# Optimization experiments

Hardware: AMD Instinct MI355X
Metric: run time of the kernel (lower is better)

Reference implementation:

```python
import jax, jax.numpy as jnp
import numpy as np

N = 50000
E = 800000
IN_C, HID, OUT_C = 512, 256, 128


def gcn_conv(x, edge_index, W, b, num_nodes):
    # PyG GCNConv: add self-loops, symmetric normalization, linear-then-aggregate.
    h = x @ W  # [N, out]
    src = jnp.concatenate([edge_index[0], jnp.arange(num_nodes)])
    dst = jnp.concatenate([edge_index[1], jnp.arange(num_nodes)])
    ones = jnp.ones(src.shape[0], dtype=x.dtype)
    deg = jax.ops.segment_sum(ones, dst, num_segments=num_nodes)  # in-degree incl. self-loop
    dinv = jax.lax.rsqrt(deg)  # deg >= 1 thanks to self-loops
    norm = dinv[src] * dinv[dst]  # [E+N]
    msg = h[src] * norm[:, None]  # gather + scale
    out = jax.ops.segment_sum(msg, dst, num_segments=num_nodes)  # scatter-add
    return out + b


def setup_inputs() -> dict:
    key = jax.random.key(0)
    k_x, k_e, k_w1, k_b1, k_w2, k_b2 = jax.random.split(key, 6)
    x = jax.random.normal(k_x, (N, IN_C), dtype=jnp.float32)
    edge_index = jax.random.randint(k_e, (2, E), 0, N, dtype=jnp.int64)
    s1 = 1.0 / np.sqrt(IN_C)
    s2 = 1.0 / np.sqrt(HID)
    W1 = jax.random.uniform(k_w1, (IN_C, HID), jnp.float32, -s1, s1)
    b1 = jax.random.uniform(k_b1, (HID,), jnp.float32, -s1, s1)
    W2 = jax.random.uniform(k_w2, (HID, OUT_C), jnp.float32, -s2, s2)
    b2 = jax.random.uniform(k_b2, (OUT_C,), jnp.float32, -s2, s2)
    return {"x": x, "edge_index": edge_index, "W1": W1, "b1": b1, "W2": W2, "b2": b2}


def reference(x, edge_index, W1, b1, W2, b2):
    h = gcn_conv(x, edge_index, W1, b1, N)
    h = jax.nn.relu(h)
    # dropout in eval mode == identity
    return gcn_conv(h, edge_index, W2, b2, N)
```

## Files before the change

kernel.cpp:

```cpp
#include <hip/hip_runtime.h>
#include <stdint.h>

typedef __bf16 bf16_t;
typedef bf16_t bf16x8 __attribute__((ext_vector_type(8)));
typedef bf16_t bf16x4 __attribute__((ext_vector_type(4)));
typedef bf16_t bf16x2 __attribute__((ext_vector_type(2)));
typedef float  f32x4  __attribute__((ext_vector_type(4)));

typedef __attribute__((address_space(3))) void* as3p;
typedef const __attribute__((address_space(1))) void* as1p;

#define IN_C 512
#define HID  256
#define OUTC 128

__global__ void k_prep(const float* __restrict__ x, const float* __restrict__ W1,
                       const float* __restrict__ W2, const void* __restrict__ ei,
                       int* __restrict__ flag, int* __restrict__ cnt,
                       bf16_t* __restrict__ Xb, bf16_t* __restrict__ W1t,
                       bf16_t* __restrict__ W2t, int n, int mpad) {
  int t = blockIdx.x * blockDim.x + threadIdx.x;
  const int NC = mpad * 64;
  if (t < NC) {
    int r = t >> 6, c8 = t & 63;
    bf16x8 o;
    if (r < n) {
      const float4* px = (const float4*)(x + (size_t)r * IN_C);
      float4 a = px[c8 * 2];
      float4 b = px[c8 * 2 + 1];
      o[0] = (bf16_t)a.x; o[1] = (bf16_t)a.y; o[2] = (bf16_t)a.z; o[3] = (bf16_t)a.w;
      o[4] = (bf16_t)b.x; o[5] = (bf16_t)b.y; o[6] = (bf16_t)b.z; o[7] = (bf16_t)b.w;
    } else {
      for (int i = 0; i < 8; ++i) o[i] = (bf16_t)0.0f;
    }
    *(bf16x8*)(Xb + (size_t)r * IN_C + c8 * 8) = o;
    return;
  }
  int u = t - NC;
  if (u < IN_C * HID) {
    W1t[(size_t)(u & 255) * IN_C + (u >> 8)] = (bf16_t)W1[u];
    return;
  }
  u -= IN_C * HID;
  if (u < HID * OUTC) {
    W2t[(size_t)(u & 127) * HID + (u >> 7)] = (bf16_t)W2[u];
    return;
  }
  u -= HID * OUTC;
  if (u < n) {
    cnt[u] = 0;
    return;
  }
  if (u == n) {
    const long long* p = (const long long*)ei;
    int ok = 1;
    for (int i = 0; i < 64; ++i) {
      long long v = p[i];
      if (v < 0 || v >= n) ok = 0;
    }
    *flag = ok;
  }
}

__global__ void k_hist(const void* __restrict__ ei, const int* __restrict__ flag,
                       int* __restrict__ cnt, int E) {
  int e = blockIdx.x * blockDim.x + threadIdx.x;
  if (e >= E) return;
  int d;
  if (*flag) d = (int)((const long long*)ei)[(size_t)E + e];
  else       d = ((const int*)ei)[E + e];
  atomicAdd(&cnt[d], 1);
}

__global__ void k_scan1(const int* __restrict__ cnt, int* __restrict__ ex,
                        int* __restrict__ part, float* __restrict__ dinv, int n) {
  __shared__ int sh[256];
  int i = blockIdx.x * 256 + threadIdx.x;
  int v = (i < n) ? cnt[i] : 0;
  if (i < n) dinv[i] = rsqrtf((float)v + 1.0f);
  sh[threadIdx.x] = v;
  __syncthreads();
  int val = v;
  for (int off = 1; off < 256; off <<= 1) {
    int t = (threadIdx.x >= off) ? sh[threadIdx.x - off] : 0;
    __syncthreads();
    val += t;
    sh[threadIdx.x] = val;
    __syncthreads();
  }
  if (i < n) ex[i] = val - v;
  if (threadIdx.x == 255) part[blockIdx.x] = val;
}

__global__ void k_scan23(int* __restrict__ rs, const int* __restrict__ part,
                         int* __restrict__ cur, int n, int Etot) {
  __shared__ int sh[256];
  const int b = blockIdx.x, t = threadIdx.x;
  int p = 0;
  for (int j = t; j < b; j += 256) p += part[j];
  sh[t] = p;
  __syncthreads();
  for (int off = 128; off > 0; off >>= 1) {
    if (t < off) sh[t] += sh[t + off];
    __syncthreads();
  }
  int base = sh[0];
  int i = b * 256 + t;
  if (i < n) {
    int r = rs[i] + base;
    rs[i] = r;
    cur[i] = r;
  }
  if (i == 0) rs[n] = Etot;
}

__global__ void k_fill(const void* __restrict__ ei, const int* __restrict__ flag,
                       int* __restrict__ cur, int2* __restrict__ csrw,
                       const float* __restrict__ dinv, int E) {
  int e = blockIdx.x * blockDim.x + threadIdx.x;
  if (e >= E) return;
  int s, d;
  if (*flag) {
    const long long* p = (const long long*)ei;
    s = (int)p[e];
    d = (int)p[(size_t)E + e];
  } else {
    const int* p = (const int*)ei;
    s = p[e];
    d = p[E + e];
  }
  int pos = atomicAdd(&cur[d], 1);
  int2 v;
  v.x = s;
  v.y = __float_as_int(dinv[s]);
  csrw[pos] = v;
}

__global__ __launch_bounds__(256, 3) void k_gemm(const bf16_t* __restrict__ A,
                                                 const bf16_t* __restrict__ Bt,
                                                 bf16_t* __restrict__ C,
                                                 int Kdim, int Ncols) {
  __shared__ bf16_t As[128 * 32];
  __shared__ bf16_t Bs[128 * 32];
  const int bm = blockIdx.x, bn = blockIdx.y;
  const int tid = threadIdx.x;
  const int wave = tid >> 6, lane = tid & 63;
  const int wm = (wave >> 1) * 64, wn = (wave & 1) * 64;
  const int quad = lane >> 4, l16 = lane & 15;

  const size_t abase = (size_t)bm * 128 * Kdim;
  const size_t bbase = (size_t)bn * 128 * Kdim;

  f32x4 acc[4][4];
#pragma unroll
  for (int i = 0; i < 4; ++i)
#pragma unroll
    for (int j = 0; j < 4; ++j)
#pragma unroll
      for (int r = 0; r < 4; ++r) acc[i][j][r] = 0.0f;

  for (int kk = 0; kk < Kdim; kk += 32) {
#pragma unroll
    for (int i = 0; i < 2; ++i) {
      int g = i * 256 + tid;
      int row = g >> 2, col = (g & 3) * 8;
      const bf16_t* ga = A + abase + (size_t)row * Kdim + kk + col;
      __builtin_amdgcn_global_load_lds((as1p)ga,
                                       (as3p)(&As[(i * 256 + wave * 64) * 8]), 16, 0, 0);
      const bf16_t* gb = Bt + bbase + (size_t)row * Kdim + kk + col;
      __builtin_amdgcn_global_load_lds((as1p)gb,
                                       (as3p)(&Bs[(i * 256 + wave * 64) * 8]), 16, 0, 0);
    }
    __syncthreads();
    bf16x8 af[4], bf[4];
#pragma unroll
    for (int i = 0; i < 4; ++i)
      af[i] = *(const bf16x8*)(&As[(wm + i * 16 + l16) * 32 + quad * 8]);
#pragma unroll
    for (int j = 0; j < 4; ++j)
      bf[j] = *(const bf16x8*)(&Bs[(wn + j * 16 + l16) * 32 + quad * 8]);
#pragma unroll
    for (int i = 0; i < 4; ++i)
#pragma unroll
      for (int j = 0; j < 4; ++j)
        acc[i][j] = __builtin_amdgcn_mfma_f32_16x16x32_bf16(af[i], bf[j], acc[i][j], 0, 0, 0);
    __syncthreads();
  }

#pragma unroll
  for (int i = 0; i < 4; ++i) {
#pragma unroll
    for (int j = 0; j < 4; ++j) {
      int col = bn * 128 + wn + j * 16 + l16;
      int row0 = bm * 128 + wm + i * 16 + quad * 4;
#pragma unroll
      for (int r = 0; r < 4; ++r)
        C[(size_t)(row0 + r) * Ncols + col] = (bf16_t)acc[i][j][r];
    }
  }
}

__global__ void k_agg_l1(const bf16_t* __restrict__ H, const int* __restrict__ rs,
                         const int2* __restrict__ csrw, const float* __restrict__ dinv,
                         const float* __restrict__ b1, bf16_t* __restrict__ R,
                         int n, int mpad) {
  int d = blockIdx.x * 4 + (threadIdx.x >> 6);
  if (d >= mpad) return;
  int lane = threadIdx.x & 63;
  if (d >= n) {
    bf16x4 z;
    z[0] = (bf16_t)0.0f; z[1] = (bf16_t)0.0f; z[2] = (bf16_t)0.0f; z[3] = (bf16_t)0.0f;
    *(bf16x4*)(R + (size_t)d * HID + lane * 4) = z;
    return;
  }
  int e0 = rs[d], e1 = rs[d + 1];
  float acc[4][4];
  for (int k = 0; k < 4; ++k)
    for (int c = 0; c < 4; ++c) acc[k][c] = 0.f;
  int e = e0;
  for (; e + 8 <= e1; e += 8) {
    int2 cw[8];
    bf16x4 h[8];
#pragma unroll
    for (int u = 0; u < 8; ++u) cw[u] = csrw[e + u];
#pragma unroll
    for (int u = 0; u < 8; ++u)
      h[u] = *(const bf16x4*)(H + (size_t)cw[u].x * HID + lane * 4);
#pragma unroll
    for (int u = 0; u < 8; ++u) {
      float w = __int_as_float(cw[u].y);
#pragma unroll
      for (int c = 0; c < 4; ++c) acc[u & 3][c] += w * (float)h[u][c];
    }
  }
  for (; e < e1; ++e) {
    int2 cw = csrw[e];
    float w = __int_as_float(cw.y);
    bf16x4 hx = *(const bf16x4*)(H + (size_t)cw.x * HID + lane * 4);
#pragma unroll
    for (int c = 0; c < 4; ++c) acc[0][c] += w * (float)hx[c];
  }
  float dd = dinv[d];
  float dv2 = dd * dd;
  bf16x4 hs = *(const bf16x4*)(H + (size_t)d * HID + lane * 4);
  float4 bb = ((const float4*)b1)[lane];
  float a0 = (acc[0][0] + acc[1][0]) + (acc[2][0] + acc[3][0]);
  float a1 = (acc[0][1] + acc[1][1]) + (acc[2][1] + acc[3][1]);
  float a2 = (acc[0][2] + acc[1][2]) + (acc[2][2] + acc[3][2]);
  float a3 = (acc[0][3] + acc[1][3]) + (acc[2][3] + acc[3][3]);
  float v0 = fmaxf(a0 * dd + dv2 * (float)hs[0] + bb.x, 0.f);
  float v1 = fmaxf(a1 * dd + dv2 * (float)hs[1] + bb.y, 0.f);
  float v2 = fmaxf(a2 * dd + dv2 * (float)hs[2] + bb.z, 0.f);
  float v3 = fmaxf(a3 * dd + dv2 * (float)hs[3] + bb.w, 0.f);
  bf16x4 o;
  o[0] = (bf16_t)v0; o[1] = (bf16_t)v1; o[2] = (bf16_t)v2; o[3] = (bf16_t)v3;
  *(bf16x4*)(R + (size_t)d * HID + lane * 4) = o;
}

__global__ void k_agg_l2(const bf16_t* __restrict__ H, const int* __restrict__ rs,
                         const int2* __restrict__ csrw, const float* __restrict__ dinv,
                         const float* __restrict__ b2, float* __restrict__ out, int n) {
  int d = blockIdx.x * 4 + (threadIdx.x >> 6);
  if (d >= n) return;
  int lane = threadIdx.x & 63;
  int e0 = rs[d], e1 = rs[d + 1];
  float acc[4][2];
  for (int k = 0; k < 4; ++k) { acc[k][0] = 0.f; acc[k][1] = 0.f; }
  int e = e0;
  for (; e + 8 <= e1; e += 8) {
    int2 cw[8];
    bf16x2 h[8];
#pragma unroll
    for (int u = 0; u < 8; ++u) cw[u] = csrw[e + u];
#pragma unroll
    for (int u = 0; u < 8; ++u)
      h[u] = *(const bf16x2*)(H + (size_t)cw[u].x * OUTC + lane * 2);
#pragma unroll
    for (int u = 0; u < 8; ++u) {
      float w = __int_as_float(cw[u].y);
      acc[u & 3][0] += w * (float)h[u][0];
      acc[u & 3][1] += w * (float)h[u][1];
    }
  }
  for (; e < e1; ++e) {
    int2 cw = csrw[e];
    float w = __int_as_float(cw.y);
    bf16x2 hx = *(const bf16x2*)(H + (size_t)cw.x * OUTC + lane * 2);
    acc[0][0] += w * (float)hx[0];
    acc[0][1] += w * (float)hx[1];
  }
  float a0 = (acc[0][0] + acc[1][0]) + (acc[2][0] + acc[3][0]);
  float a1 = (acc[0][1] + acc[1][1]) + (acc[2][1] + acc[3][1]);
  float dd = dinv[d];
  float dv2 = dd * dd;
  bf16x2 hs = *(const bf16x2*)(H + (size_t)d * OUTC + lane * 2);
  float2 bb = ((const float2*)b2)[lane];
  float2 o;
  o.x = a0 * dd + dv2 * (float)hs[0] + bb.x;
  o.y = a1 * dd + dv2 * (float)hs[1] + bb.y;
  ((float2*)(out + (size_t)d * OUTC))[lane] = o;
}

extern "C" void kernel_launch(void* const* d_in, const int* in_sizes, int n_in,
                              void* d_out, int out_size, void* d_ws, size_t ws_size,
                              hipStream_t stream) {
  const float* x  = (const float*)d_in[0];
  const void*  ei = d_in[1];
  const float* W1 = (const float*)d_in[2];
  const float* b1 = (const float*)d_in[3];
  const float* W2 = (const float*)d_in[4];
  const float* b2 = (const float*)d_in[5];

  const int n = in_sizes[0] / IN_C;
  const int E = in_sizes[1] / 2;
  const int mpad = (n + 127) & ~127;

  char* w = (char*)d_ws;
  size_t off = 0;
  auto alloc = [&](size_t bytes) -> void* {
    void* p = w + off;
    off = (off + bytes + 255) & ~(size_t)255;
    return p;
  };

  int*    flag = (int*)alloc(4);
  int*    cnt  = (int*)alloc((size_t)n * 4);
  float*  dinv = (float*)alloc((size_t)n * 4);
  int*    rs   = (int*)alloc((size_t)(n + 1) * 4);
  int*    cur  = (int*)alloc((size_t)n * 4);
  int*    part = (int*)alloc(1024);
  int2*   csrw = (int2*)alloc((size_t)E * 8);
  bf16_t* Xb   = (bf16_t*)alloc((size_t)mpad * IN_C * 2);
  bf16_t* W1t  = (bf16_t*)alloc((size_t)HID * IN_C * 2);
  bf16_t* W2t  = (bf16_t*)alloc((size_t)OUTC * HID * 2);
  bf16_t* H1b  = (bf16_t*)alloc((size_t)mpad * HID * 2);
  bf16_t* R1b  = (bf16_t*)alloc((size_t)mpad * HID * 2);
  bf16_t* H2b  = (bf16_t*)alloc((size_t)mpad * OUTC * 2);
  (void)ws_size; (void)n_in; (void)out_size;

  const int nb = (n + 255) / 256;
  const int prepT = mpad * 64 + IN_C * HID + HID * OUTC + n + 1;

  k_prep<<<(prepT + 255) / 256, 256, 0, stream>>>(x, W1, W2, ei, flag, cnt,
                                                  Xb, W1t, W2t, n, mpad);
  k_hist<<<(E + 255) / 256, 256, 0, stream>>>(ei, flag, cnt, E);
  k_scan1<<<nb, 256, 0, stream>>>(cnt, rs, part, dinv, n);
  k_scan23<<<nb, 256, 0, stream>>>(rs, part, cur, n, E);
  k_fill<<<(E + 255) / 256, 256, 0, stream>>>(ei, flag, cur, csrw, dinv, E);

  k_gemm<<<dim3(mpad / 128, HID / 128), 256, 0, stream>>>(Xb, W1t, H1b, IN_C, HID);
  k_agg_l1<<<(mpad + 3) / 4, 256, 0, stream>>>(H1b, rs, csrw, dinv, b1, R1b, n, mpad);
  k_gemm<<<dim3(mpad / 128, OUTC / 128), 256, 0, stream>>>(R1b, W2t, H2b, HID, OUTC);
  k_agg_l2<<<(n + 3) / 4, 256, 0, stream>>>(H2b, rs, csrw, dinv, b2, (float*)d_out, n);
}
```

Baseline: 397.6 us.

## Fuse fp32-to-bf16 input conversion into first GEMM and persist aggregation kernels

```diff
diff --git a/kernel.cpp b/kernel.cpp
--- a/kernel.cpp
+++ b/kernel.cpp
@@ -14,34 +14,16 @@
 #define HID  256
 #define OUTC 128
 
-__global__ void k_prep(const float* __restrict__ x, const float* __restrict__ W1,
-                       const float* __restrict__ W2, const void* __restrict__ ei,
-                       int* __restrict__ flag, int* __restrict__ cnt,
-                       bf16_t* __restrict__ Xb, bf16_t* __restrict__ W1t,
-                       bf16_t* __restrict__ W2t, int n, int mpad) {
+__global__ void k_prep(const float* __restrict__ W1, const float* __restrict__ W2,
+                       const void* __restrict__ ei, int* __restrict__ flag,
+                       int* __restrict__ cnt, bf16_t* __restrict__ W1t,
+                       bf16_t* __restrict__ W2t, int n) {
   int t = blockIdx.x * blockDim.x + threadIdx.x;
-  const int NC = mpad * 64;
-  if (t < NC) {
-    int r = t >> 6, c8 = t & 63;
-    bf16x8 o;
-    if (r < n) {
-      const float4* px = (const float4*)(x + (size_t)r * IN_C);
-      float4 a = px[c8 * 2];
-      float4 b = px[c8 * 2 + 1];
-      o[0] = (bf16_t)a.x; o[1] = (bf16_t)a.y; o[2] = (bf16_t)a.z; o[3] = (bf16_t)a.w;
-      o[4] = (bf16_t)b.x; o[5] = (bf16_t)b.y; o[6] = (bf16_t)b.z; o[7] = (bf16_t)b.w;
-    } else {
-      for (int i = 0; i < 8; ++i) o[i] = (bf16_t)0.0f;
-    }
-    *(bf16x8*)(Xb + (size_t)r * IN_C + c8 * 8) = o;
+  if (t < IN_C * HID) {
+    W1t[(size_t)(t & 255) * IN_C + (t >> 8)] = (bf16_t)W1[t];
     return;
   }
-  int u = t - NC;
-  if (u < IN_C * HID) {
-    W1t[(size_t)(u & 255) * IN_C + (u >> 8)] = (bf16_t)W1[u];
-    return;
-  }
-  u -= IN_C * HID;
+  int u = t - IN_C * HID;
   if (u < HID * OUTC) {
     W2t[(size_t)(u & 127) * HID + (u >> 7)] = (bf16_t)W2[u];
     return;
@@ -136,6 +118,81 @@
   csrw[pos] = v;
 }
 
+__global__ __launch_bounds__(512, 2) void k_gemm1(const float* __restrict__ A,
+                                                  const bf16_t* __restrict__ Bt,
+                                                  bf16_t* __restrict__ C, int n) {
+  __shared__ float  As[128 * 32];
+  __shared__ bf16_t Bs[256 * 32];
+  const int bm = blockIdx.x;
+  const int tid = threadIdx.x;
+  const int wave = tid >> 6, lane = tid & 63;
+  const int wm = (wave >> 2) * 64, wn = (wave & 3) * 64;
+  const int quad = lane >> 4, l16 = lane & 15;
+  const int rowclamp = n - 1;
+
+  f32x4 acc[4][4];
+#pragma unroll
+  for (int i = 0; i < 4; ++i)
+#pragma unroll
+    for (int j = 0; j < 4; ++j)
+#pragma unroll
+      for (int r = 0; r < 4; ++r) acc[i][j][r] = 0.0f;
+
+  for (int kk = 0; kk < IN_C; kk += 32) {
+#pragma unroll
+    for (int i = 0; i < 2; ++i) {
+      int g = i * 512 + tid;
+      int rat = g >> 3, ca = g & 7;
+      int garow = bm * 128 + rat;
+      if (garow > rowclamp) garow = rowclamp;
+      const float* srcA = A + (size_t)garow * IN_C + kk + ((ca ^ (rat & 7)) << 2);
+      __builtin_amdgcn_global_load_lds((as1p)srcA,
+                                       (as3p)(As + (size_t)(i * 512 + wave * 64) * 4), 16, 0, 0);
+      int rbt = g >> 2, cb = g & 3;
+      const bf16_t* srcB = Bt + (size_t)rbt * IN_C + kk + ((cb ^ ((rbt >> 1) & 3)) << 3);
+      __builtin_amdgcn_global_load_lds((as1p)srcB,
+                                       (as3p)(Bs + (size_t)(i * 512 + wave * 64) * 8), 16, 0, 0);
+    }
+    __syncthreads();
+    bf16x8 af[4], bfr[4];
+#pragma unroll
+    for (int i = 0; i < 4; ++i) {
+      int ra = wm + i * 16 + l16;
+      const float* base = As + ra * 32;
+      int s = ra & 7;
+      f32x4 v0 = *(const f32x4*)(base + (((quad * 2) ^ s) << 2));
+      f32x4 v1 = *(const f32x4*)(base + (((quad * 2 + 1) ^ s) << 2));
+      bf16x8 a;
+      a[0] = (bf16_t)v0[0]; a[1] = (bf16_t)v0[1]; a[2] = (bf16_t)v0[2]; a[3] = (bf16_t)v0[3];
+      a[4] = (bf16_t)v1[0]; a[5] = (bf16_t)v1[1]; a[6] = (bf16_t)v1[2]; a[7] = (bf16_t)v1[3];
+      af[i] = a;
+    }
+#pragma unroll
+    for (int j = 0; j < 4; ++j) {
+      int rb = wn + j * 16 + l16;
+      bfr[j] = *(const bf16x8*)(Bs + rb * 32 + ((quad ^ ((rb >> 1) & 3)) << 3));
+    }
+#pragma unroll
+    for (int i = 0; i < 4; ++i)
+#pragma unroll
+      for (int j = 0; j < 4; ++j)
+        acc[i][j] = __builtin_amdgcn_mfma_f32_16x16x32_bf16(af[i], bfr[j], acc[i][j], 0, 0, 0);
+    __syncthreads();
+  }
+
+#pragma unroll
+  for (int i = 0; i < 4; ++i) {
+#pragma unroll
+    for (int j = 0; j < 4; ++j) {
+      int col = wn + j * 16 + l16;
+      int row0 = bm * 128 + wm + i * 16 + quad * 4;
+#pragma unroll
+      for (int r = 0; r < 4; ++r)
+        C[(size_t)(row0 + r) * HID + col] = (bf16_t)acc[i][j][r];
+    }
+  }
+}
+
 __global__ __launch_bounds__(256, 3) void k_gemm(const bf16_t* __restrict__ A,
                                                  const bf16_t* __restrict__ Bt,
                                                  bf16_t* __restrict__ C,
@@ -200,105 +257,116 @@
   }
 }
 
-__global__ void k_agg_l1(const bf16_t* __restrict__ H, const int* __restrict__ rs,
-                         const int2* __restrict__ csrw, const float* __restrict__ dinv,
-                         const float* __restrict__ b1, bf16_t* __restrict__ R,
-                         int n, int mpad) {
-  int d = blockIdx.x * 4 + (threadIdx.x >> 6);
-  if (d >= mpad) return;
-  int lane = threadIdx.x & 63;
-  if (d >= n) {
-    bf16x4 z;
-    z[0] = (bf16_t)0.0f; z[1] = (bf16_t)0.0f; z[2] = (bf16_t)0.0f; z[3] = (bf16_t)0.0f;
-    *(bf16x4*)(R + (size_t)d * HID + lane * 4) = z;
-    return;
-  }
-  int e0 = rs[d], e1 = rs[d + 1];
-  float acc[4][4];
-  for (int k = 0; k < 4; ++k)
-    for (int c = 0; c < 4; ++c) acc[k][c] = 0.f;
-  int e = e0;
-  for (; e + 8 <= e1; e += 8) {
-    int2 cw[8];
-    bf16x4 h[8];
-#pragma unroll
-    for (int u = 0; u < 8; ++u) cw[u] = csrw[e + u];
-#pragma unroll
-    for (int u = 0; u < 8; ++u)
-      h[u] = *(const bf16x4*)(H + (size_t)cw[u].x * HID + lane * 4);
-#pragma unroll
-    for (int u = 0; u < 8; ++u) {
-      float w = __int_as_float(cw[u].y);
-#pragma unroll
-      for (int c = 0; c < 4; ++c) acc[u & 3][c] += w * (float)h[u][c];
-    }
-  }
-  for (; e < e1; ++e) {
-    int2 cw = csrw[e];
-    float w = __int_as_float(cw.y);
-    bf16x4 hx = *(const bf16x4*)(H + (size_t)cw.x * HID + lane * 4);
-#pragma unroll
-    for (int c = 0; c < 4; ++c) acc[0][c] += w * (float)hx[c];
-  }
-  float dd = dinv[d];
-  float dv2 = dd * dd;
-  bf16x4 hs = *(const bf16x4*)(H + (size_t)d * HID + lane * 4);
-  float4 bb = ((const float4*)b1)[lane];
-  float a0 = (acc[0][0] + acc[1][0]) + (acc[2][0] + acc[3][0]);
-  float a1 = (acc[0][1] + acc[1][1]) + (acc[2][1] + acc[3][1]);
-  float a2 = (acc[0][2] + acc[1][2]) + (acc[2][2] + acc[3][2]);
-  float a3 = (acc[0][3] + acc[1][3]) + (acc[2][3] + acc[3][3]);
-  float v0 = fmaxf(a0 * dd + dv2 * (float)hs[0] + bb.x, 0.f);
-  float v1 = fmaxf(a1 * dd + dv2 * (float)hs[1] + bb.y, 0.f);
-  float v2 = fmaxf(a2 * dd + dv2 * (float)hs[2] + bb.z, 0.f);
-  float v3 = fmaxf(a3 * dd + dv2 * (float)hs[3] + bb.w, 0.f);
-  bf16x4 o;
-  o[0] = (bf16_t)v0; o[1] = (bf16_t)v1; o[2] = (bf16_t)v2; o[3] = (bf16_t)v3;
-  *(bf16x4*)(R + (size_t)d * HID + lane * 4) = o;
-}
-
-__global__ void k_agg_l2(const bf16_t* __restrict__ H, const int* __restrict__ rs,
-                         const int2* __restrict__ csrw, const float* __restrict__ dinv,
-                         const float* __restrict__ b2, float* __restrict__ out, int n) {
-  int d = blockIdx.x * 4 + (threadIdx.x >> 6);
-  if (d >= n) return;
-  int lane = threadIdx.x & 63;
-  int e0 = rs[d], e1 = rs[d + 1];
-  float acc[4][2];
-  for (int k = 0; k < 4; ++k) { acc[k][0] = 0.f; acc[k][1] = 0.f; }
-  int e = e0;
-  for (; e + 8 <= e1; e += 8) {
-    int2 cw[8];
-    bf16x2 h[8];
-#pragma unroll
-    for (int u = 0; u < 8; ++u) cw[u] = csrw[e + u];
-#pragma unroll
-    for (int u = 0; u < 8; ++u)
-      h[u] = *(const bf16x2*)(H + (size_t)cw[u].x * OUTC + lane * 2);
-#pragma unroll
-    for (int u = 0; u < 8; ++u) {
-      float w = __int_as_float(cw[u].y);
-      acc[u & 3][0] += w * (float)h[u][0];
-      acc[u & 3][1] += w * (float)h[u][1];
-    }
-  }
-  for (; e < e1; ++e) {
-    int2 cw = csrw[e];
-    float w = __int_as_float(cw.y);
-    bf16x2 hx = *(const bf16x2*)(H + (size_t)cw.x * OUTC + lane * 2);
-    acc[0][0] += w * (float)hx[0];
-    acc[0][1] += w * (float)hx[1];
-  }
-  float a0 = (acc[0][0] + acc[1][0]) + (acc[2][0] + acc[3][0]);
-  float a1 = (acc[0][1] + acc[1][1]) + (acc[2][1] + acc[3][1]);
-  float dd = dinv[d];
-  float dv2 = dd * dd;
-  bf16x2 hs = *(const bf16x2*)(H + (size_t)d * OUTC + lane * 2);
-  float2 bb = ((const float2*)b2)[lane];
-  float2 o;
-  o.x = a0 * dd + dv2 * (float)hs[0] + bb.x;
-  o.y = a1 * dd + dv2 * (float)hs[1] + bb.y;
-  ((float2*)(out + (size_t)d * OUTC))[lane] = o;
+__global__ __launch_bounds__(256, 8) void k_agg_l1(const bf16_t* __restrict__ H,
+                                                   const int* __restrict__ rs,
+                                                   const int2* __restrict__ csrw,
+                                                   const float* __restrict__ dinv,
+                                                   const float* __restrict__ b1,
+                                                   bf16_t* __restrict__ R,
+                                                   int n, int mpad) {
+  const int lane = threadIdx.x & 63;
+  const int nw = gridDim.x << 2;
+  const float4 bb = ((const float4*)b1)[lane];
+  for (int d = (blockIdx.x << 2) + (threadIdx.x >> 6); d < mpad; d += nw) {
+    if (d >= n) {
+      bf16x4 z;
+      z[0] = (bf16_t)0.0f; z[1] = (bf16_t)0.0f; z[2] = (bf16_t)0.0f; z[3] = (bf16_t)0.0f;
+      *(bf16x4*)(R + (size_t)d * HID + lane * 4) = z;
+      continue;
+    }
+    int e0 = rs[d], e1 = rs[d + 1];
+    float acc[4][4];
+#pragma unroll
+    for (int k = 0; k < 4; ++k)
+#pragma unroll
+      for (int c = 0; c < 4; ++c) acc[k][c] = 0.f;
+    int e = e0;
+    for (; e + 8 <= e1; e += 8) {
+      int2 cw[8];
+      bf16x4 h[8];
+#pragma unroll
+      for (int u = 0; u < 8; ++u) cw[u] = csrw[e + u];
+#pragma unroll
+      for (int u = 0; u < 8; ++u)
+        h[u] = *(const bf16x4*)(H + (size_t)cw[u].x * HID + lane * 4);
+#pragma unroll
+      for (int u = 0; u < 8; ++u) {
+        float w = __int_as_float(cw[u].y);
+#pragma unroll
+        for (int c = 0; c < 4; ++c) acc[u & 3][c] += w * (float)h[u][c];
+      }
+    }
+    for (; e < e1; ++e) {
+      int2 cw = csrw[e];
+      float w = __int_as_float(cw.y);
+      bf16x4 hx = *(const bf16x4*)(H + (size_t)cw.x * HID + lane * 4);
+#pragma unroll
+      for (int c = 0; c < 4; ++c) acc[0][c] += w * (float)hx[c];
+    }
+    float dd = dinv[d];
+    float dv2 = dd * dd;
+    bf16x4 hs = *(const bf16x4*)(H + (size_t)d * HID + lane * 4);
+    float a0 = (acc[0][0] + acc[1][0]) + (acc[2][0] + acc[3][0]);
+    float a1 = (acc[0][1] + acc[1][1]) + (acc[2][1] + acc[3][1]);
+    float a2 = (acc[0][2] + acc[1][2]) + (acc[2][2] + acc[3][2]);
+    float a3 = (acc[0][3] + acc[1][3]) + (acc[2][3] + acc[3][3]);
+    float v0 = fmaxf(a0 * dd + dv2 * (float)hs[0] + bb.x, 0.f);
+    float v1 = fmaxf(a1 * dd + dv2 * (float)hs[1] + bb.y, 0.f);
+    float v2 = fmaxf(a2 * dd + dv2 * (float)hs[2] + bb.z, 0.f);
+    float v3 = fmaxf(a3 * dd + dv2 * (float)hs[3] + bb.w, 0.f);
+    bf16x4 o;
+    o[0] = (bf16_t)v0; o[1] = (bf16_t)v1; o[2] = (bf16_t)v2; o[3] = (bf16_t)v3;
+    *(bf16x4*)(R + (size_t)d * HID + lane * 4) = o;
+  }
+}
+
+__global__ __launch_bounds__(256, 8) void k_agg_l2(const bf16_t* __restrict__ H,
+                                                   const int* __restrict__ rs,
+                                                   const int2* __restrict__ csrw,
+                                                   const float* __restrict__ dinv,
+                                                   const float* __restrict__ b2,
+                                                   float* __restrict__ out, int n) {
+  const int lane = threadIdx.x & 63;
+  const int nw = gridDim.x << 2;
+  const float2 bb = ((const float2*)b2)[lane];
+  for (int d = (blockIdx.x << 2) + (threadIdx.x >> 6); d < n; d += nw) {
+    int e0 = rs[d], e1 = rs[d + 1];
+    float acc[4][2];
+#pragma unroll
+    for (int k = 0; k < 4; ++k) { acc[k][0] = 0.f; acc[k][1] = 0.f; }
+    int e = e0;
+    for (; e + 8 <= e1; e += 8) {
+      int2 cw[8];
+      bf16x2 h[8];
+#pragma unroll
+      for (int u = 0; u < 8; ++u) cw[u] = csrw[e + u];
+#pragma unroll
+      for (int u = 0; u < 8; ++u)
+        h[u] = *(const bf16x2*)(H + (size_t)cw[u].x * OUTC + lane * 2);
+#pragma unroll
+      for (int u = 0; u < 8; ++u) {
+        float w = __int_as_float(cw[u].y);
+        acc[u & 3][0] += w * (float)h[u][0];
+        acc[u & 3][1] += w * (float)h[u][1];
+      }
+    }
+    for (; e < e1; ++e) {
+      int2 cw = csrw[e];
+      float w = __int_as_float(cw.y);
+      bf16x2 hx = *(const bf16x2*)(H + (size_t)cw.x * OUTC + lane * 2);
+      acc[0][0] += w * (float)hx[0];
+      acc[0][1] += w * (float)hx[1];
+    }
+    float a0 = (acc[0][0] + acc[1][0]) + (acc[2][0] + acc[3][0]);
+    float a1 = (acc[0][1] + acc[1][1]) + (acc[2][1] + acc[3][1]);
+    float dd = dinv[d];
+    float dv2 = dd * dd;
+    bf16x2 hs = *(const bf16x2*)(H + (size_t)d * OUTC + lane * 2);
+    float2 o;
+    o.x = a0 * dd + dv2 * (float)hs[0] + bb.x;
+    o.y = a1 * dd + dv2 * (float)hs[1] + bb.y;
+    ((float2*)(out + (size_t)d * OUTC))[lane] = o;
+  }
 }
 
 extern "C" void kernel_launch(void* const* d_in, const int* in_sizes, int n_in,
@@ -330,7 +398,6 @@
   int*    cur  = (int*)alloc((size_t)n * 4);
   int*    part = (int*)alloc(1024);
   int2*   csrw = (int2*)alloc((size_t)E * 8);
-  bf16_t* Xb   = (bf16_t*)alloc((size_t)mpad * IN_C * 2);
   bf16_t* W1t  = (bf16_t*)alloc((size_t)HID * IN_C * 2);
   bf16_t* W2t  = (bf16_t*)alloc((size_t)OUTC * HID * 2);
   bf16_t* H1b  = (bf16_t*)alloc((size_t)mpad * HID * 2);
@@ -339,17 +406,16 @@
   (void)ws_size; (void)n_in; (void)out_size;
 
   const int nb = (n + 255) / 256;
-  const int prepT = mpad * 64 + IN_C * HID + HID * OUTC + n + 1;
-
-  k_prep<<<(prepT + 255) / 256, 256, 0, stream>>>(x, W1, W2, ei, flag, cnt,
-                                                  Xb, W1t, W2t, n, mpad);
+  const int prepT = IN_C * HID + HID * OUTC + n + 1;
+
+  k_prep<<<(prepT + 255) / 256, 256, 0, stream>>>(W1, W2, ei, flag, cnt, W1t, W2t, n);
   k_hist<<<(E + 255) / 256, 256, 0, stream>>>(ei, flag, cnt, E);
   k_scan1<<<nb, 256, 0, stream>>>(cnt, rs, part, dinv, n);
   k_scan23<<<nb, 256, 0, stream>>>(rs, part, cur, n, E);
   k_fill<<<(E + 255) / 256, 256, 0, stream>>>(ei, flag, cur, csrw, dinv, E);
 
-  k_gemm<<<dim3(mpad / 128, HID / 128), 256, 0, stream>>>(Xb, W1t, H1b, IN_C, HID);
-  k_agg_l1<<<(mpad + 3) / 4, 256, 0, stream>>>(H1b, rs, csrw, dinv, b1, R1b, n, mpad);
-  k_gemm<<<dim3(mpad / 128, OUTC / 128), 256, 0, stream>>>(R1b, W2t, H2b, HID, OUTC);
-  k_agg_l2<<<(n + 3) / 4, 256, 0, stream>>>(H2b, rs, csrw, dinv, b2, (float*)d_out, n);
-}
+  k_gemm1<<<mpad / 128, 512, 0, stream>>>(x, W1t, H1b, n);
+  k_agg_l1<<<2048, 256, 0, stream>>>(H1b, rs, csrw, dinv, b1, R1b, n, mpad);
+  k_gemm<<<dim3(mpad / 128, 1), 256, 0, stream>>>(R1b, W2t, H2b, HID, OUTC);
+  k_agg_l2<<<2048, 256, 0, stream>>>(H2b, rs, csrw, dinv, b2, (float*)d_out, n);
+}
```

New measurement: 406.1 us. 1.02x slower.
